# Optimization experiments

Hardware: AMD Instinct MI355X
Metric: run time of the kernel (lower is better)

## Reference

```python
import jax, jax.numpy as jnp
import numpy as np

PATCH = 16
EMBED = 384
BINS = 32
LN_EPS = 1e-5


def setup_inputs() -> dict:
    key = jax.random.key(0)
    k1, k2 = jax.random.split(key, 2)
    images = jax.random.uniform(k1, (64, 3, 224, 224), dtype=jnp.float32)  # pixels in [0,1]
    proj_w = jax.random.normal(k2, (EMBED, 3, PATCH, PATCH), dtype=jnp.float32) * 0.02  # OIHW
    proj_b = jnp.zeros((EMBED,), jnp.float32)
    ln_gamma = jnp.ones((EMBED,), jnp.float32)
    ln_beta = jnp.zeros((EMBED,), jnp.float32)
    return {"images": images, "proj_w": proj_w, "proj_b": proj_b,
            "ln_gamma": ln_gamma, "ln_beta": ln_beta}


def _patch_entropy(images, patch_size):
    # images: (B, C, H, W) in [0,1]
    B, C, H, W = images.shape
    gH, gW = H // patch_size, W // patch_size
    gray = images.mean(axis=1)  # (B, H, W)
    # non-overlapping patches -> (B, N, P*P)
    patches = gray.reshape(B, gH, patch_size, gW, patch_size)
    patches = patches.transpose(0, 1, 3, 2, 4).reshape(B, gH * gW, patch_size * patch_size)
    # quantize to 32 bins (floor, matching torch .long() on non-negative values)
    q = jnp.clip(patches * (BINS - 1), 0, BINS - 1).astype(jnp.int32)
    one_hot = jax.nn.one_hot(q, BINS, dtype=jnp.float32)      # (B, N, P*P, 32)
    hist = one_hot.sum(axis=2)                                 # (B, N, 32)
    prob = hist / jnp.maximum(hist.sum(axis=-1, keepdims=True), 1e-8)
    log_prob = jnp.log2(prob + 1e-10)
    entropy = -(prob * log_prob).sum(axis=-1)                  # (B, N)
    return entropy / np.float32(np.log2(BINS))


def reference(images, proj_w, proj_b, ln_gamma, ln_beta):
    p = PATCH
    B, C, H, W = images.shape
    gH, gW = H // p, W // p
    entropy = _patch_entropy(images, p)
    # patch-embed conv: kernel=stride=patch_size, VALID padding
    x = jax.lax.conv_general_dilated(
        images, proj_w, window_strides=(p, p), padding='VALID',
        dimension_numbers=('NCHW', 'OIHW', 'NCHW'))            # (B, D, gH, gW)
    x = x + proj_b[None, :, None, None]
    x = x.transpose(0, 2, 3, 1).reshape(B, gH * gW, -1)        # (B, N, D)
    mu = x.mean(axis=-1, keepdims=True)
    var = x.var(axis=-1, keepdims=True)                        # biased, like torch LayerNorm
    x = (x - mu) / jnp.sqrt(var + LN_EPS) * ln_gamma + ln_beta
    return x, entropy
```

## Files before the change

### kernel.cpp

```cpp
#include <hip/hip_runtime.h>

#define BATCH 64
#define GH 14
#define GW 14
#define NPATCH (GH*GW)
#define M_ROWS (BATCH*NPATCH)
#define KDIM 768
#define DDIM 384
#define HW (224*224)

typedef __attribute__((ext_vector_type(8))) short s16x8;
typedef __attribute__((ext_vector_type(4))) float f32x4;
typedef __attribute__((ext_vector_type(4))) unsigned short u16x4;

__device__ __forceinline__ unsigned short f2bf(float f) {
    unsigned int u = __float_as_uint(f);
    u += 0x7fff + ((u >> 16) & 1);
    return (unsigned short)(u >> 16);
}

__device__ __forceinline__ void load_lds16(const void* g, void* l) {
    __builtin_amdgcn_global_load_lds(
        (const __attribute__((address_space(1))) unsigned int*)g,
        (__attribute__((address_space(3))) unsigned int*)l, 16, 0, 0);
}

__global__ __launch_bounds__(256) void patch_kernel(const float* __restrict__ img,
                                                    const float* __restrict__ w,
                                                    unsigned short* __restrict__ A,
                                                    unsigned short* __restrict__ W,
                                                    float* __restrict__ ent) {
    if (blockIdx.x >= 3136) {
        int t = (blockIdx.x - 3136) * 256 + threadIdx.x;
        float4 v = ((const float4*)w)[t];
        u16x4 o = { f2bf(v.x), f2bf(v.y), f2bf(v.z), f2bf(v.w) };
        *(u16x4*)(W + t * 4) = o;
        return;
    }
    __shared__ int hist[4][32];
    const int lane = threadIdx.x & 63;
    const int wave = threadIdx.x >> 6;
    const int p = blockIdx.x * 4 + wave;
    const int b = p / NPATCH;
    const int n = p - b * NPATCH;
    const int ph = n / GW, pw = n - ph * GW;

    if (lane < 32) hist[wave][lane] = 0;
    __syncthreads();

    const int r = lane >> 2;
    const int cc = (lane & 3) * 4;
    const float* base = img + (size_t)b * (3 * HW) + (ph * 16 + r) * 224 + pw * 16 + cc;

    float4 v0 = *(const float4*)(base);
    float4 v1 = *(const float4*)(base + HW);
    float4 v2 = *(const float4*)(base + 2 * HW);

    unsigned short* arow = A + (size_t)p * KDIM;
    u16x4 o0 = { f2bf(v0.x), f2bf(v0.y), f2bf(v0.z), f2bf(v0.w) };
    u16x4 o1 = { f2bf(v1.x), f2bf(v1.y), f2bf(v1.z), f2bf(v1.w) };
    u16x4 o2 = { f2bf(v2.x), f2bf(v2.y), f2bf(v2.z), f2bf(v2.w) };
    *(u16x4*)(arow + 0 * 256 + lane * 4) = o0;
    *(u16x4*)(arow + 1 * 256 + lane * 4) = o1;
    *(u16x4*)(arow + 2 * 256 + lane * 4) = o2;

    float g[4] = { (v0.x + v1.x + v2.x) / 3.0f,
                   (v0.y + v1.y + v2.y) / 3.0f,
                   (v0.z + v1.z + v2.z) / 3.0f,
                   (v0.w + v1.w + v2.w) / 3.0f };
#pragma unroll
    for (int j = 0; j < 4; ++j) {
        int bin = (int)(g[j] * 31.0f);
        bin = bin < 0 ? 0 : (bin > 31 ? 31 : bin);
        atomicAdd(&hist[wave][bin], 1);
    }
    __syncthreads();

    float t = 0.0f;
    if (lane < 32) {
        float pr = (float)hist[wave][lane] * (1.0f / 256.0f);
        t = -pr * log2f(pr + 1e-10f);
    }
#pragma unroll
    for (int off = 32; off; off >>= 1) t += __shfl_xor(t, off);
    if (lane == 0) ent[p] = t * (1.0f / 5.0f);
}

__global__ __launch_bounds__(384) void gemm_ln_kernel(const unsigned short* __restrict__ A,
                                                      const unsigned short* __restrict__ Bt,
                                                      const float* __restrict__ bias,
                                                      const float* __restrict__ gamma,
                                                      const float* __restrict__ beta,
                                                      float* __restrict__ C) {
    __shared__ __align__(16) unsigned short SH[(64 + 384) * 64];
    __shared__ float sred[64], sred2[64], smean[64], srstd[64];
    unsigned short* As = SH;
    unsigned short* Bs = SH + 64 * 64;

    const int tid  = threadIdx.x;
    const int lane = tid & 63;
    const int w    = tid >> 6;
    const int quad = lane >> 4;
    const int cl   = lane & 15;
    const int rowBase = blockIdx.x * 64;

    if (tid < 64) { sred[tid] = 0.0f; sred2[tid] = 0.0f; }

    f32x4 acc[4][4] = {};

    for (int kt = 0; kt < KDIM; kt += 64) {
#pragma unroll
        for (int i = 0; i < 10; ++i) {
            int cb = i * 384 + w * 64;
            if (i == 9 && cb >= 3584 - 64 + 64) {  }
            if (i == 9 && w >= 2) break;
            int c = (i == 9) ? (3456 + tid) : (cb + lane);
            if (c < 512) {
                int r  = c >> 3, kss = c & 7;
                int ksg = kss ^ (r & 7);
                load_lds16(A + (size_t)(rowBase + r) * KDIM + kt + ksg * 8,
                           (unsigned short*)SH + c * 8);
            } else {
                int cc2 = c - 512;
                int n  = cc2 >> 3, kss = cc2 & 7;
                int ksg = kss ^ (n & 7);
                load_lds16(Bt + (size_t)n * KDIM + kt + ksg * 8,
                           (unsigned short*)SH + c * 8);
            }
        }
        __syncthreads();
#pragma unroll
        for (int ks = 0; ks < 2; ++ks) {
            const int sw = (ks * 4 + quad) ^ (cl & 7);
            s16x8 a_frag[4], b_frag[4];
#pragma unroll
            for (int i = 0; i < 4; ++i) {
                a_frag[i] = *(const s16x8*)(As + ((i * 16 + cl) * 8 + sw) * 8);
                b_frag[i] = *(const s16x8*)(Bs + ((w * 64 + i * 16 + cl) * 8 + sw) * 8);
            }
#pragma unroll
            for (int i = 0; i < 4; ++i)
#pragma unroll
                for (int j = 0; j < 4; ++j)
                    acc[i][j] = __builtin_amdgcn_mfma_f32_16x16x32_bf16(
                        a_frag[i], b_frag[j], acc[i][j], 0, 0, 0);
        }
        __syncthreads();
    }

    float bv[4], gv[4], btv[4];
#pragma unroll
    for (int j = 0; j < 4; ++j) {
        int col = w * 64 + j * 16 + cl;
        bv[j] = bias[col]; gv[j] = gamma[col]; btv[j] = beta[col];
    }

#pragma unroll
    for (int i = 0; i < 4; ++i) {
#pragma unroll
        for (int r = 0; r < 4; ++r) {
            float s1 = 0.0f, s2 = 0.0f;
#pragma unroll
            for (int j = 0; j < 4; ++j) {
                float v = acc[i][j][r] + bv[j];
                s1 += v; s2 += v * v;
            }
#pragma unroll
            for (int off = 1; off < 16; off <<= 1) {
                s1 += __shfl_xor(s1, off);
                s2 += __shfl_xor(s2, off);
            }
            if (cl == 0) {
                int row = i * 16 + quad * 4 + r;
                atomicAdd(&sred[row], s1);
                atomicAdd(&sred2[row], s2);
            }
        }
    }
    __syncthreads();
    if (tid < 64) {
        float mu  = sred[tid] * (1.0f / (float)DDIM);
        float var = sred2[tid] * (1.0f / (float)DDIM) - mu * mu;
        smean[tid] = mu;
        srstd[tid] = rsqrtf(var + 1e-5f);
    }
    __syncthreads();

#pragma unroll
    for (int i = 0; i < 4; ++i) {
#pragma unroll
        for (int r = 0; r < 4; ++r) {
            int row = i * 16 + quad * 4 + r;
            float mu = smean[row], rs = srstd[row];
            float* crow = C + (size_t)(rowBase + row) * DDIM;
#pragma unroll
            for (int j = 0; j < 4; ++j)
                crow[w * 64 + j * 16 + cl] = (acc[i][j][r] + bv[j] - mu) * rs * gv[j] + btv[j];
        }
    }
}

extern "C" void kernel_launch(void* const* d_in, const int* in_sizes, int n_in,
                              void* d_out, int out_size, void* d_ws, size_t ws_size,
                              hipStream_t stream) {
    const float* img = (const float*)d_in[0];
    const float* pw  = (const float*)d_in[1];
    const float* pb  = (const float*)d_in[2];
    const float* gam = (const float*)d_in[3];
    const float* bet = (const float*)d_in[4];
    float* out = (float*)d_out;

    unsigned short* Abf = (unsigned short*)d_ws;
    unsigned short* Wbf = (unsigned short*)((char*)d_ws + 19267584);
    float* ent = out + (size_t)M_ROWS * DDIM;

    hipLaunchKernelGGL(patch_kernel,   dim3(3424), dim3(256), 0, stream,
                       img, pw, Abf, Wbf, ent);
    hipLaunchKernelGGL(gemm_ln_kernel, dim3(196),  dim3(384), 0, stream,
                       Abf, Wbf, pb, gam, bet, out);
}
```

Before: 113.6 us.

## Fuse patch extraction and entropy into the GEMM+LayerNorm kernel

Removes the intermediate bf16 patch matrix: the GEMM kernel now reads fp32 image pixels directly, converts them to bf16 and stages them in LDS with register prefetch of the next K tile. The per-patch entropy histogram is computed inside the same kernel before the GEMM starts. Weight casting moves to its own small kernel. The intent is to cut the global write and re-read of the A matrix and one large launch. In exchange, the 196-block GEMM grid now also carries the histogram work, and direct LDS loads are replaced by register-staged stores with an extra barrier per K step.

```diff
diff --git a/kernel.cpp b/kernel.cpp
--- a/kernel.cpp
+++ b/kernel.cpp
@@ -19,124 +19,142 @@
     return (unsigned short)(u >> 16);
 }
 
-__device__ __forceinline__ void load_lds16(const void* g, void* l) {
-    __builtin_amdgcn_global_load_lds(
-        (const __attribute__((address_space(1))) unsigned int*)g,
-        (__attribute__((address_space(3))) unsigned int*)l, 16, 0, 0);
-}
-
-__global__ __launch_bounds__(256) void patch_kernel(const float* __restrict__ img,
-                                                    const float* __restrict__ w,
-                                                    unsigned short* __restrict__ A,
-                                                    unsigned short* __restrict__ W,
+__device__ __forceinline__ s16x8 cvt8(float4 lo, float4 hi) {
+    s16x8 o;
+    o[0] = (short)f2bf(lo.x); o[1] = (short)f2bf(lo.y);
+    o[2] = (short)f2bf(lo.z); o[3] = (short)f2bf(lo.w);
+    o[4] = (short)f2bf(hi.x); o[5] = (short)f2bf(hi.y);
+    o[6] = (short)f2bf(hi.z); o[7] = (short)f2bf(hi.w);
+    return o;
+}
+
+__global__ __launch_bounds__(256) void wcast_kernel(const float* __restrict__ w,
+                                                    unsigned short* __restrict__ W) {
+    int t = blockIdx.x * 256 + threadIdx.x;
+    float4 v = ((const float4*)w)[t];
+    u16x4 o = { f2bf(v.x), f2bf(v.y), f2bf(v.z), f2bf(v.w) };
+    *(u16x4*)(W + t * 4) = o;
+}
+
+__global__ __launch_bounds__(384) void fused_kernel(const float* __restrict__ img,
+                                                    const unsigned short* __restrict__ Bt,
+                                                    const float* __restrict__ bias,
+                                                    const float* __restrict__ gamma,
+                                                    const float* __restrict__ beta,
+                                                    float* __restrict__ C,
                                                     float* __restrict__ ent) {
-    if (blockIdx.x >= 3136) {
-        int t = (blockIdx.x - 3136) * 256 + threadIdx.x;
-        float4 v = ((const float4*)w)[t];
-        u16x4 o = { f2bf(v.x), f2bf(v.y), f2bf(v.z), f2bf(v.w) };
-        *(u16x4*)(W + t * 4) = o;
-        return;
-    }
-    __shared__ int hist[4][32];
-    const int lane = threadIdx.x & 63;
-    const int wave = threadIdx.x >> 6;
-    const int p = blockIdx.x * 4 + wave;
-    const int b = p / NPATCH;
-    const int n = p - b * NPATCH;
-    const int ph = n / GW, pw = n - ph * GW;
-
-    if (lane < 32) hist[wave][lane] = 0;
-    __syncthreads();
-
-    const int r = lane >> 2;
-    const int cc = (lane & 3) * 4;
-    const float* base = img + (size_t)b * (3 * HW) + (ph * 16 + r) * 224 + pw * 16 + cc;
-
-    float4 v0 = *(const float4*)(base);
-    float4 v1 = *(const float4*)(base + HW);
-    float4 v2 = *(const float4*)(base + 2 * HW);
-
-    unsigned short* arow = A + (size_t)p * KDIM;
-    u16x4 o0 = { f2bf(v0.x), f2bf(v0.y), f2bf(v0.z), f2bf(v0.w) };
-    u16x4 o1 = { f2bf(v1.x), f2bf(v1.y), f2bf(v1.z), f2bf(v1.w) };
-    u16x4 o2 = { f2bf(v2.x), f2bf(v2.y), f2bf(v2.z), f2bf(v2.w) };
-    *(u16x4*)(arow + 0 * 256 + lane * 4) = o0;
-    *(u16x4*)(arow + 1 * 256 + lane * 4) = o1;
-    *(u16x4*)(arow + 2 * 256 + lane * 4) = o2;
-
-    float g[4] = { (v0.x + v1.x + v2.x) / 3.0f,
-                   (v0.y + v1.y + v2.y) / 3.0f,
-                   (v0.z + v1.z + v2.z) / 3.0f,
-                   (v0.w + v1.w + v2.w) / 3.0f };
-#pragma unroll
-    for (int j = 0; j < 4; ++j) {
-        int bin = (int)(g[j] * 31.0f);
-        bin = bin < 0 ? 0 : (bin > 31 ? 31 : bin);
-        atomicAdd(&hist[wave][bin], 1);
-    }
-    __syncthreads();
-
-    float t = 0.0f;
-    if (lane < 32) {
-        float pr = (float)hist[wave][lane] * (1.0f / 256.0f);
-        t = -pr * log2f(pr + 1e-10f);
-    }
-#pragma unroll
-    for (int off = 32; off; off >>= 1) t += __shfl_xor(t, off);
-    if (lane == 0) ent[p] = t * (1.0f / 5.0f);
-}
-
-__global__ __launch_bounds__(384) void gemm_ln_kernel(const unsigned short* __restrict__ A,
-                                                      const unsigned short* __restrict__ Bt,
-                                                      const float* __restrict__ bias,
-                                                      const float* __restrict__ gamma,
-                                                      const float* __restrict__ beta,
-                                                      float* __restrict__ C) {
-    __shared__ __align__(16) unsigned short SH[(64 + 384) * 64];
+    __shared__ __align__(16) unsigned short As[64 * 64];
+    __shared__ __align__(16) unsigned short Bs[384 * 64];
+    __shared__ int hist[6][32];
     __shared__ float sred[64], sred2[64], smean[64], srstd[64];
-    unsigned short* As = SH;
-    unsigned short* Bs = SH + 64 * 64;
 
     const int tid  = threadIdx.x;
     const int lane = tid & 63;
-    const int w    = tid >> 6;
+    const int wv   = tid >> 6;
     const int quad = lane >> 4;
     const int cl   = lane & 15;
     const int rowBase = blockIdx.x * 64;
 
     if (tid < 64) { sred[tid] = 0.0f; sred2[tid] = 0.0f; }
 
+    const int r1  = tid >> 3, ksg = tid & 7;
+    const int sA1 = r1 * 64 + (ksg ^ (r1 & 7)) * 8;
+    const int r2  = r1 + 48;
+    const int sA2 = r2 * 64 + (ksg ^ (r2 & 7)) * 8;
+    const float *pA1, *pA2;
+    {
+        int p = rowBase + r1, b = p / NPATCH, n = p - b * NPATCH;
+        int ph = n / GW, pw_ = n - ph * GW;
+        pA1 = img + (size_t)b * (3 * HW) + (ph * 16 + (ksg >> 1)) * 224 + pw_ * 16 + (ksg & 1) * 8;
+        p = rowBase + r2; b = p / NPATCH; n = p - b * NPATCH;
+        ph = n / GW; pw_ = n - ph * GW;
+        pA2 = img + (size_t)b * (3 * HW) + (ph * 16 + (ksg >> 1)) * 224 + pw_ * 16 + (ksg & 1) * 8;
+    }
+    const unsigned short* pB0 = Bt + (size_t)(tid >> 3) * KDIM + (tid & 7) * 8;
+    const int sB = (tid >> 3) * 64 + ((tid & 7) ^ ((tid >> 3) & 7)) * 8;
+
+    s16x8 breg[8];
+#pragma unroll
+    for (int i = 0; i < 8; ++i)
+        breg[i] = *(const s16x8*)(pB0 + (size_t)i * (48 * KDIM));
+    float4 a1lo = *(const float4*)(pA1);
+    float4 a1hi = *(const float4*)(pA1 + 4);
+    float4 a2lo, a2hi;
+    if (tid < 128) { a2lo = *(const float4*)(pA2); a2hi = *(const float4*)(pA2 + 4); }
+
+    {
+        const int pr  = lane >> 2;
+        const int cc4 = (lane & 3) * 4;
+        int p0 = rowBase + wv, b0 = p0 / NPATCH, n0i = p0 - b0 * NPATCH;
+        int ph0 = n0i / GW, pw0 = n0i - ph0 * GW;
+        const float* bp = img + (size_t)b0 * (3 * HW) + (ph0 * 16 + pr) * 224 + pw0 * 16 + cc4;
+        float4 c0 = *(const float4*)(bp);
+        float4 c1 = *(const float4*)(bp + HW);
+        float4 c2 = *(const float4*)(bp + 2 * HW);
+        for (int pp = wv; pp < 64; pp += 6) {
+            float4 n0, n1, n2;
+            if (pp + 6 < 64) {
+                int p = rowBase + pp + 6, b = p / NPATCH, n = p - b * NPATCH;
+                int ph = n / GW, pw_ = n - ph * GW;
+                const float* np = img + (size_t)b * (3 * HW) + (ph * 16 + pr) * 224 + pw_ * 16 + cc4;
+                n0 = *(const float4*)(np);
+                n1 = *(const float4*)(np + HW);
+                n2 = *(const float4*)(np + 2 * HW);
+            }
+            if (lane < 32) hist[wv][lane] = 0;
+            asm volatile("s_waitcnt lgkmcnt(0)" ::: "memory");
+            float g[4] = { (c0.x + c1.x + c2.x) / 3.0f, (c0.y + c1.y + c2.y) / 3.0f,
+                           (c0.z + c1.z + c2.z) / 3.0f, (c0.w + c1.w + c2.w) / 3.0f };
+#pragma unroll
+            for (int j = 0; j < 4; ++j) {
+                int bin = (int)(g[j] * 31.0f);
+                bin = bin < 0 ? 0 : (bin > 31 ? 31 : bin);
+                atomicAdd(&hist[wv][bin], 1);
+            }
+            asm volatile("s_waitcnt lgkmcnt(0)" ::: "memory");
+            float t = 0.0f;
+            if (lane < 32) {
+                float prb = (float)hist[wv][lane] * (1.0f / 256.0f);
+                t = -prb * log2f(prb + 1e-10f);
+            }
+#pragma unroll
+            for (int off = 32; off; off >>= 1) t += __shfl_xor(t, off);
+            if (lane == 0) ent[rowBase + pp] = t * (1.0f / 5.0f);
+            c0 = n0; c1 = n1; c2 = n2;
+        }
+    }
+
+    *(s16x8*)(As + sA1) = cvt8(a1lo, a1hi);
+    if (tid < 128) *(s16x8*)(As + sA2) = cvt8(a2lo, a2hi);
+#pragma unroll
+    for (int i = 0; i < 8; ++i)
+        *(s16x8*)(Bs + sB + i * (48 * 64)) = breg[i];
+    __syncthreads();
+
     f32x4 acc[4][4] = {};
-
-    for (int kt = 0; kt < KDIM; kt += 64) {
-#pragma unroll
-        for (int i = 0; i < 10; ++i) {
-            int cb = i * 384 + w * 64;
-            if (i == 9 && cb >= 3584 - 64 + 64) {  }
-            if (i == 9 && w >= 2) break;
-            int c = (i == 9) ? (3456 + tid) : (cb + lane);
-            if (c < 512) {
-                int r  = c >> 3, kss = c & 7;
-                int ksg = kss ^ (r & 7);
-                load_lds16(A + (size_t)(rowBase + r) * KDIM + kt + ksg * 8,
-                           (unsigned short*)SH + c * 8);
-            } else {
-                int cc2 = c - 512;
-                int n  = cc2 >> 3, kss = cc2 & 7;
-                int ksg = kss ^ (n & 7);
-                load_lds16(Bt + (size_t)n * KDIM + kt + ksg * 8,
-                           (unsigned short*)SH + c * 8);
-            }
-        }
-        __syncthreads();
+    for (int kt = 0; kt < 12; ++kt) {
+        if (kt < 11) {
+            const int kn = kt + 1;
+            const float* pa = pA1 + (kn >> 2) * HW + (kn & 3) * (4 * 224);
+            a1lo = *(const float4*)(pa);
+            a1hi = *(const float4*)(pa + 4);
+            if (tid < 128) {
+                const float* pa2 = pA2 + (kn >> 2) * HW + (kn & 3) * (4 * 224);
+                a2lo = *(const float4*)(pa2);
+                a2hi = *(const float4*)(pa2 + 4);
+            }
+#pragma unroll
+            for (int i = 0; i < 8; ++i)
+                breg[i] = *(const s16x8*)(pB0 + (size_t)i * (48 * KDIM) + kn * 64);
+        }
 #pragma unroll
         for (int ks = 0; ks < 2; ++ks) {
             const int sw = (ks * 4 + quad) ^ (cl & 7);
             s16x8 a_frag[4], b_frag[4];
 #pragma unroll
             for (int i = 0; i < 4; ++i) {
-                a_frag[i] = *(const s16x8*)(As + ((i * 16 + cl) * 8 + sw) * 8);
-                b_frag[i] = *(const s16x8*)(Bs + ((w * 64 + i * 16 + cl) * 8 + sw) * 8);
+                a_frag[i] = *(const s16x8*)(As + (i * 16 + cl) * 64 + sw * 8);
+                b_frag[i] = *(const s16x8*)(Bs + (wv * 64 + i * 16 + cl) * 64 + sw * 8);
             }
 #pragma unroll
             for (int i = 0; i < 4; ++i)
@@ -146,12 +164,20 @@
                         a_frag[i], b_frag[j], acc[i][j], 0, 0, 0);
         }
         __syncthreads();
+        if (kt < 11) {
+            *(s16x8*)(As + sA1) = cvt8(a1lo, a1hi);
+            if (tid < 128) *(s16x8*)(As + sA2) = cvt8(a2lo, a2hi);
+#pragma unroll
+            for (int i = 0; i < 8; ++i)
+                *(s16x8*)(Bs + sB + i * (48 * 64)) = breg[i];
+        }
+        __syncthreads();
     }
 
     float bv[4], gv[4], btv[4];
 #pragma unroll
     for (int j = 0; j < 4; ++j) {
-        int col = w * 64 + j * 16 + cl;
+        int col = wv * 64 + j * 16 + cl;
         bv[j] = bias[col]; gv[j] = gamma[col]; btv[j] = beta[col];
     }
 
@@ -195,7 +221,7 @@
             float* crow = C + (size_t)(rowBase + row) * DDIM;
 #pragma unroll
             for (int j = 0; j < 4; ++j)
-                crow[w * 64 + j * 16 + cl] = (acc[i][j][r] + bv[j] - mu) * rs * gv[j] + btv[j];
+                crow[wv * 64 + j * 16 + cl] = (acc[i][j][r] + bv[j] - mu) * rs * gv[j] + btv[j];
         }
     }
 }
@@ -210,12 +236,10 @@
     const float* bet = (const float*)d_in[4];
     float* out = (float*)d_out;
 
-    unsigned short* Abf = (unsigned short*)d_ws;
-    unsigned short* Wbf = (unsigned short*)((char*)d_ws + 19267584);
+    unsigned short* Wbf = (unsigned short*)d_ws;
     float* ent = out + (size_t)M_ROWS * DDIM;
 
-    hipLaunchKernelGGL(patch_kernel,   dim3(3424), dim3(256), 0, stream,
-                       img, pw, Abf, Wbf, ent);
-    hipLaunchKernelGGL(gemm_ln_kernel, dim3(196),  dim3(384), 0, stream,
-                       Abf, Wbf, pb, gam, bet, out);
-}
+    hipLaunchKernelGGL(wcast_kernel, dim3(288), dim3(256), 0, stream, pw, Wbf);
+    hipLaunchKernelGGL(fused_kernel, dim3(196), dim3(384), 0, stream,
+                       img, Wbf, pb, gam, bet, out, ent);
+}
```

New measurement: 118.2 us. +4.0%, slower.

## Split fused GEMM+LayerNorm into smaller-tile double-buffered GEMM and separate LN kernel

Applied to the files above, without the earlier changes.

The fused GEMM+LN kernel ran only 196 blocks, each owning a full 64x384 row tile, so most CUs on the GPU sat idle. It is replaced by a GEMM with 32x128 tiles over 1176 blocks, using double-buffered LDS loads to overlap global-to-LDS copies with MFMA work. LayerNorm moves to a separate kernel that re-reads and rewrites the fp32 output. This trades an extra launch and an extra pass over the ~38MB output for much higher parallelism, and the smaller tiles give less operand reuse.

```diff
diff --git a/kernel.cpp b/kernel.cpp
--- a/kernel.cpp
+++ b/kernel.cpp
@@ -86,117 +86,122 @@
     if (lane == 0) ent[p] = t * (1.0f / 5.0f);
 }
 
-__global__ __launch_bounds__(384) void gemm_ln_kernel(const unsigned short* __restrict__ A,
-                                                      const unsigned short* __restrict__ Bt,
-                                                      const float* __restrict__ bias,
-                                                      const float* __restrict__ gamma,
-                                                      const float* __restrict__ beta,
-                                                      float* __restrict__ C) {
-    __shared__ __align__(16) unsigned short SH[(64 + 384) * 64];
-    __shared__ float sred[64], sred2[64], smean[64], srstd[64];
-    unsigned short* As = SH;
-    unsigned short* Bs = SH + 64 * 64;
+__global__ __launch_bounds__(256) void gemm_kernel(const unsigned short* __restrict__ A,
+                                                   const unsigned short* __restrict__ Bt,
+                                                   const float* __restrict__ bias,
+                                                   float* __restrict__ C) {
+    __shared__ __align__(16) unsigned short SH[2][1280 * 8];
 
     const int tid  = threadIdx.x;
     const int lane = tid & 63;
-    const int w    = tid >> 6;
+    const int wv   = tid >> 6;
     const int quad = lane >> 4;
     const int cl   = lane & 15;
-    const int rowBase = blockIdx.x * 64;
-
-    if (tid < 64) { sred[tid] = 0.0f; sred2[tid] = 0.0f; }
-
-    f32x4 acc[4][4] = {};
-
-    for (int kt = 0; kt < KDIM; kt += 64) {
-#pragma unroll
-        for (int i = 0; i < 10; ++i) {
-            int cb = i * 384 + w * 64;
-            if (i == 9 && cb >= 3584 - 64 + 64) {  }
-            if (i == 9 && w >= 2) break;
-            int c = (i == 9) ? (3456 + tid) : (cb + lane);
-            if (c < 512) {
-                int r  = c >> 3, kss = c & 7;
-                int ksg = kss ^ (r & 7);
-                load_lds16(A + (size_t)(rowBase + r) * KDIM + kt + ksg * 8,
-                           (unsigned short*)SH + c * 8);
+    const int rowBase = (blockIdx.x / 3) * 32;
+    const int colBase = (blockIdx.x % 3) * 128;
+
+    const unsigned short* srcs[5];
+    {
+#pragma unroll
+        for (int i = 0; i < 5; ++i) {
+            int c = i * 256 + tid;
+            if (c < 256) {
+                int r = c >> 3, kss = c & 7, ksg = kss ^ (r & 7);
+                srcs[i] = A + (size_t)(rowBase + r) * KDIM + ksg * 8;
             } else {
-                int cc2 = c - 512;
-                int n  = cc2 >> 3, kss = cc2 & 7;
-                int ksg = kss ^ (n & 7);
-                load_lds16(Bt + (size_t)n * KDIM + kt + ksg * 8,
-                           (unsigned short*)SH + c * 8);
+                int cc = c - 256;
+                int n = cc >> 3, kss = cc & 7, ksg = kss ^ (n & 7);
+                srcs[i] = Bt + (size_t)(colBase + n) * KDIM + ksg * 8;
             }
         }
-        __syncthreads();
+    }
+    const int dstOff = tid * 8;
+
+#pragma unroll
+    for (int i = 0; i < 5; ++i)
+        load_lds16(srcs[i], &SH[0][i * 2048 + dstOff]);
+    __syncthreads();
+
+    f32x4 acc[2][2] = {};
+#pragma unroll
+    for (int kt = 0; kt < 12; ++kt) {
+        const int cur = kt & 1;
+        if (kt < 11) {
+#pragma unroll
+            for (int i = 0; i < 5; ++i)
+                load_lds16(srcs[i] + (kt + 1) * 64, &SH[cur ^ 1][i * 2048 + dstOff]);
+        }
+        const unsigned short* As = SH[cur];
+        const unsigned short* Bs = SH[cur] + 2048;
 #pragma unroll
         for (int ks = 0; ks < 2; ++ks) {
             const int sw = (ks * 4 + quad) ^ (cl & 7);
-            s16x8 a_frag[4], b_frag[4];
-#pragma unroll
-            for (int i = 0; i < 4; ++i) {
-                a_frag[i] = *(const s16x8*)(As + ((i * 16 + cl) * 8 + sw) * 8);
-                b_frag[i] = *(const s16x8*)(Bs + ((w * 64 + i * 16 + cl) * 8 + sw) * 8);
-            }
-#pragma unroll
-            for (int i = 0; i < 4; ++i)
-#pragma unroll
-                for (int j = 0; j < 4; ++j)
+            s16x8 af[2], bf[2];
+#pragma unroll
+            for (int i = 0; i < 2; ++i)
+                af[i] = *(const s16x8*)(As + ((i * 16 + cl) * 8 + sw) * 8);
+#pragma unroll
+            for (int j = 0; j < 2; ++j)
+                bf[j] = *(const s16x8*)(Bs + ((wv * 32 + j * 16 + cl) * 8 + sw) * 8);
+#pragma unroll
+            for (int i = 0; i < 2; ++i)
+#pragma unroll
+                for (int j = 0; j < 2; ++j)
                     acc[i][j] = __builtin_amdgcn_mfma_f32_16x16x32_bf16(
-                        a_frag[i], b_frag[j], acc[i][j], 0, 0, 0);
+                        af[i], bf[j], acc[i][j], 0, 0, 0);
         }
         __syncthreads();
     }
 
-    float bv[4], gv[4], btv[4];
-#pragma unroll
-    for (int j = 0; j < 4; ++j) {
-        int col = w * 64 + j * 16 + cl;
-        bv[j] = bias[col]; gv[j] = gamma[col]; btv[j] = beta[col];
-    }
-
-#pragma unroll
-    for (int i = 0; i < 4; ++i) {
+    float bv[2];
+#pragma unroll
+    for (int j = 0; j < 2; ++j)
+        bv[j] = bias[colBase + wv * 32 + j * 16 + cl];
+#pragma unroll
+    for (int i = 0; i < 2; ++i)
 #pragma unroll
         for (int r = 0; r < 4; ++r) {
-            float s1 = 0.0f, s2 = 0.0f;
-#pragma unroll
-            for (int j = 0; j < 4; ++j) {
-                float v = acc[i][j][r] + bv[j];
-                s1 += v; s2 += v * v;
-            }
-#pragma unroll
-            for (int off = 1; off < 16; off <<= 1) {
-                s1 += __shfl_xor(s1, off);
-                s2 += __shfl_xor(s2, off);
-            }
-            if (cl == 0) {
-                int row = i * 16 + quad * 4 + r;
-                atomicAdd(&sred[row], s1);
-                atomicAdd(&sred2[row], s2);
-            }
-        }
-    }
-    __syncthreads();
-    if (tid < 64) {
-        float mu  = sred[tid] * (1.0f / (float)DDIM);
-        float var = sred2[tid] * (1.0f / (float)DDIM) - mu * mu;
-        smean[tid] = mu;
-        srstd[tid] = rsqrtf(var + 1e-5f);
-    }
-    __syncthreads();
-
-#pragma unroll
-    for (int i = 0; i < 4; ++i) {
-#pragma unroll
-        for (int r = 0; r < 4; ++r) {
-            int row = i * 16 + quad * 4 + r;
-            float mu = smean[row], rs = srstd[row];
-            float* crow = C + (size_t)(rowBase + row) * DDIM;
-#pragma unroll
-            for (int j = 0; j < 4; ++j)
-                crow[w * 64 + j * 16 + cl] = (acc[i][j][r] + bv[j] - mu) * rs * gv[j] + btv[j];
-        }
+            int row = rowBase + i * 16 + quad * 4 + r;
+            float* crow = C + (size_t)row * DDIM + colBase + wv * 32;
+#pragma unroll
+            for (int j = 0; j < 2; ++j)
+                crow[j * 16 + cl] = acc[i][j][r] + bv[j];
+        }
+}
+
+__global__ __launch_bounds__(256) void ln_kernel(float* __restrict__ x,
+                                                 const float* __restrict__ gamma,
+                                                 const float* __restrict__ beta) {
+    const int lane = threadIdx.x & 63;
+    const int wv   = threadIdx.x >> 6;
+    const int row  = blockIdx.x * 4 + wv;
+
+    float2* px = (float2*)(x + (size_t)row * DDIM);
+    float2 v[3];
+    float s1 = 0.0f, s2 = 0.0f;
+#pragma unroll
+    for (int k = 0; k < 3; ++k) {
+        v[k] = px[lane + k * 64];
+        s1 += v[k].x + v[k].y;
+        s2 += v[k].x * v[k].x + v[k].y * v[k].y;
+    }
+#pragma unroll
+    for (int off = 1; off < 64; off <<= 1) {
+        s1 += __shfl_xor(s1, off);
+        s2 += __shfl_xor(s2, off);
+    }
+    float mu  = s1 * (1.0f / (float)DDIM);
+    float var = s2 * (1.0f / (float)DDIM) - mu * mu;
+    float rs  = rsqrtf(var + 1e-5f);
+#pragma unroll
+    for (int k = 0; k < 3; ++k) {
+        int c2 = lane + k * 64;
+        float2 g = ((const float2*)gamma)[c2];
+        float2 b = ((const float2*)beta)[c2];
+        float2 o;
+        o.x = (v[k].x - mu) * rs * g.x + b.x;
+        o.y = (v[k].y - mu) * rs * g.y + b.y;
+        px[c2] = o;
     }
 }
 
@@ -214,8 +219,10 @@
     unsigned short* Wbf = (unsigned short*)((char*)d_ws + 19267584);
     float* ent = out + (size_t)M_ROWS * DDIM;
 
-    hipLaunchKernelGGL(patch_kernel,   dim3(3424), dim3(256), 0, stream,
+    hipLaunchKernelGGL(patch_kernel, dim3(3424), dim3(256), 0, stream,
                        img, pw, Abf, Wbf, ent);
-    hipLaunchKernelGGL(gemm_ln_kernel, dim3(196),  dim3(384), 0, stream,
-                       Abf, Wbf, pb, gam, bet, out);
-}
+    hipLaunchKernelGGL(gemm_kernel,  dim3(1176), dim3(256), 0, stream,
+                       Abf, Wbf, pb, out);
+    hipLaunchKernelGGL(ln_kernel,    dim3(3136), dim3(256), 0, stream,
+                       out, gam, bet);
+}
```

After: 116.9 us. 1.03x slower.
